# Kernel tuning notes

Hardware: AMD Instinct MI355X
Metric: run time of the kernel (lower is better)

Reference implementation:

```python
import jax, jax.numpy as jnp
import numpy as np

TAU = 1.0
BETA = 1.0


def setup_inputs() -> dict:
    key = jax.random.key(0)
    n, depth = 128, 2048
    inputs = jax.random.normal(key, (1, n, n, depth), dtype=jnp.float32)
    return {"inputs": inputs}


def reference(inputs):
    # Faithful vectorized version of MaskLayer.call (original uses Python loops).
    x = inputs[0]                      # (n, n, d), channels-last feature maps
    n = x.shape[0]
    d = x.shape[2]
    # Per-channel argmax over the flattened (row-major) n*n map.
    flat_idx = jnp.argmax(x.reshape(n * n, d), axis=0)   # (d,)
    # NOTE: original code sets row = idx % n -> i_max, col = idx // n -> j_max
    # (i.e. transposed coordinates); we reproduce that exactly.
    i_max = (flat_idx % n).astype(jnp.float32)           # (d,)
    j_max = (flat_idx // n).astype(jnp.float32)          # (d,)
    i = jnp.arange(n, dtype=jnp.float32)[:, None, None]  # (n,1,1)
    j = jnp.arange(n, dtype=jnp.float32)[None, :, None]  # (1,n,1)
    l1 = jnp.abs(i - i_max) + jnp.abs(j - j_max)         # (n,n,d)
    mask = TAU * jnp.maximum(-1.0, 1.0 - BETA * l1 / n)
    return x * mask
```

## Files before the change

### kernel.cpp

```cpp
#include <hip/hip_runtime.h>

constexpr int N_  = 128;
constexpr int D_  = 2048;
constexpr int NP_ = N_ * N_;

typedef float f32x4 __attribute__((ext_vector_type(4)));

__device__ __forceinline__ unsigned int fmap(float f) {
    unsigned int b = __float_as_uint(f);
    return (b & 0x80000000u) ? ~b : (b | 0x80000000u);
}

__global__ __launch_bounds__(256)
void argmax_kernel(const float* __restrict__ x,
                   unsigned long long* __restrict__ keys) {
    const int cIdx = blockIdx.x * 256 + threadIdx.x;
    const int p0   = blockIdx.y * 64;
    const f32x4* __restrict__ x4 = (const f32x4*)x;

    unsigned long long b0 = 0, b1 = 0, b2 = 0, b3 = 0;
    #pragma unroll 8
    for (int p = p0; p < p0 + 64; ++p) {
        f32x4 v = x4[(size_t)p * (D_ / 4) + cIdx];
        unsigned long long lo = (unsigned long long)(unsigned int)(NP_ - 1 - p);
        unsigned long long k0 = ((unsigned long long)fmap(v.x) << 32) | lo;
        unsigned long long k1 = ((unsigned long long)fmap(v.y) << 32) | lo;
        unsigned long long k2 = ((unsigned long long)fmap(v.z) << 32) | lo;
        unsigned long long k3 = ((unsigned long long)fmap(v.w) << 32) | lo;
        b0 = max(b0, k0);
        b1 = max(b1, k1);
        b2 = max(b2, k2);
        b3 = max(b3, k3);
    }
    unsigned long long* k = keys + (size_t)cIdx * 4;
    atomicMax(&k[0], b0);
    atomicMax(&k[1], b1);
    atomicMax(&k[2], b2);
    atomicMax(&k[3], b3);
}

__global__ __launch_bounds__(256)
void apply_kernel(const float* __restrict__ x,
                  const unsigned long long* __restrict__ keys,
                  float* __restrict__ out) {
    const int g  = blockIdx.x * 256 + threadIdx.x;
    const int e  = g * 4;
    const int c4 = e & (D_ - 1);
    const int p  = e >> 11;
    const float fi = (float)(p >> 7);
    const float fj = (float)(p & 127);

    f32x4 v = __builtin_nontemporal_load(((const f32x4*)x) + g);

    float m[4];
    #pragma unroll
    for (int t = 0; t < 4; ++t) {
        unsigned long long k = keys[c4 + t];
        unsigned int pm = (unsigned int)(NP_ - 1) - (unsigned int)(k & 0xFFFFFFFFull);
        float imax = (float)(pm & 127);
        float jmax = (float)(pm >> 7);
        float l1 = fabsf(fi - imax) + fabsf(fj - jmax);
        m[t] = fmaxf(-1.0f, 1.0f - l1 * (1.0f / 128.0f));
    }

    f32x4 o;
    o.x = v.x * m[0];
    o.y = v.y * m[1];
    o.z = v.z * m[2];
    o.w = v.w * m[3];
    __builtin_nontemporal_store(o, ((f32x4*)out) + g);
}

extern "C" void kernel_launch(void* const* d_in, const int* in_sizes, int n_in,
                              void* d_out, int out_size, void* d_ws, size_t ws_size,
                              hipStream_t stream) {
    const float* x = (const float*)d_in[0];
    float* out = (float*)d_out;
    unsigned long long* keys = (unsigned long long*)d_ws;

    (void)hipMemsetAsync(keys, 0, D_ * sizeof(unsigned long long), stream);

    dim3 g1(2, 256);
    argmax_kernel<<<g1, dim3(256), 0, stream>>>(x, keys);

    const int total4 = NP_ * D_ / 4;
    apply_kernel<<<total4 / 256, dim3(256), 0, stream>>>(x, keys, out);
}
```

Baseline: 257.3 us.

## Replace atomic argmax with two-stage reduction and grid-stride apply kernel

Argmax partials are written per row block and then reduced in a separate small kernel. This removes the memset and 64-bit atomics, and the reduce kernel also precomputes the float max coordinates. The apply kernel becomes a grid-stride loop over 2048 blocks and uses normal rather than nontemporal loads for x, so data cached from the argmax pass may be reused. In exchange it adds an extra kernel launch and a workspace buffer for the partials.

```diff
diff --git a/kernel.cpp b/kernel.cpp
--- a/kernel.cpp
+++ b/kernel.cpp
@@ -3,8 +3,10 @@
 constexpr int N_  = 128;
 constexpr int D_  = 2048;
 constexpr int NP_ = N_ * N_;
+constexpr int YB_ = 256;
 
 typedef float f32x4 __attribute__((ext_vector_type(4)));
+typedef float f32x2 __attribute__((ext_vector_type(2)));
 
 __device__ __forceinline__ unsigned int fmap(float f) {
     unsigned int b = __float_as_uint(f);
@@ -12,15 +14,16 @@
 }
 
 __global__ __launch_bounds__(256)
-void argmax_kernel(const float* __restrict__ x,
-                   unsigned long long* __restrict__ keys) {
+void argmax_partial(const float* __restrict__ x,
+                    unsigned long long* __restrict__ partial) {
     const int cIdx = blockIdx.x * 256 + threadIdx.x;
-    const int p0   = blockIdx.y * 64;
+    const int by   = blockIdx.y;
+    const int p0   = by * (NP_ / YB_);
     const f32x4* __restrict__ x4 = (const f32x4*)x;
 
     unsigned long long b0 = 0, b1 = 0, b2 = 0, b3 = 0;
     #pragma unroll 8
-    for (int p = p0; p < p0 + 64; ++p) {
+    for (int p = p0; p < p0 + (NP_ / YB_); ++p) {
         f32x4 v = x4[(size_t)p * (D_ / 4) + cIdx];
         unsigned long long lo = (unsigned long long)(unsigned int)(NP_ - 1 - p);
         unsigned long long k0 = ((unsigned long long)fmap(v.x) << 32) | lo;
@@ -32,43 +35,49 @@
         b2 = max(b2, k2);
         b3 = max(b3, k3);
     }
-    unsigned long long* k = keys + (size_t)cIdx * 4;
-    atomicMax(&k[0], b0);
-    atomicMax(&k[1], b1);
-    atomicMax(&k[2], b2);
-    atomicMax(&k[3], b3);
+    unsigned long long* dst = partial + (size_t)by * D_ + (size_t)cIdx * 4;
+    dst[0] = b0; dst[1] = b1; dst[2] = b2; dst[3] = b3;
+}
+
+__global__ __launch_bounds__(64)
+void argmax_reduce(const unsigned long long* __restrict__ partial,
+                   f32x2* __restrict__ maxpos) {
+    const int c = blockIdx.x * 64 + threadIdx.x;
+    unsigned long long b = 0;
+    #pragma unroll 8
+    for (int by = 0; by < YB_; ++by)
+        b = max(b, partial[(size_t)by * D_ + c]);
+    unsigned int pm = (unsigned int)(NP_ - 1) - (unsigned int)(b & 0xFFFFFFFFull);
+    f32x2 mp;
+    mp.x = (float)(pm & 127);
+    mp.y = (float)(pm >> 7);
+    maxpos[c] = mp;
 }
 
 __global__ __launch_bounds__(256)
 void apply_kernel(const float* __restrict__ x,
-                  const unsigned long long* __restrict__ keys,
+                  const f32x2* __restrict__ maxpos,
                   float* __restrict__ out) {
-    const int g  = blockIdx.x * 256 + threadIdx.x;
-    const int e  = g * 4;
-    const int c4 = e & (D_ - 1);
-    const int p  = e >> 11;
-    const float fi = (float)(p >> 7);
-    const float fj = (float)(p & 127);
+    constexpr int TOTAL4 = NP_ * D_ / 4;
+    constexpr int STRIDE = 2048 * 256;
+    for (int g = blockIdx.x * 256 + threadIdx.x; g < TOTAL4; g += STRIDE) {
+        const int e  = g * 4;
+        const int c4 = e & (D_ - 1);
+        const int p  = e >> 11;
+        const float fi = (float)(p >> 7);
+        const float fj = (float)(p & 127);
 
-    f32x4 v = __builtin_nontemporal_load(((const f32x4*)x) + g);
-
-    float m[4];
-    #pragma unroll
-    for (int t = 0; t < 4; ++t) {
-        unsigned long long k = keys[c4 + t];
-        unsigned int pm = (unsigned int)(NP_ - 1) - (unsigned int)(k & 0xFFFFFFFFull);
-        float imax = (float)(pm & 127);
-        float jmax = (float)(pm >> 7);
-        float l1 = fabsf(fi - imax) + fabsf(fj - jmax);
-        m[t] = fmaxf(-1.0f, 1.0f - l1 * (1.0f / 128.0f));
+        f32x4 v = ((const f32x4*)x)[g];
+        f32x4 o;
+        #pragma unroll
+        for (int t = 0; t < 4; ++t) {
+            f32x2 mp = maxpos[c4 + t];
+            float l1 = fabsf(fi - mp.x) + fabsf(fj - mp.y);
+            float m  = fmaxf(-1.0f, 1.0f - l1 * (1.0f / 128.0f));
+            o[t] = v[t] * m;
+        }
+        __builtin_nontemporal_store(o, ((f32x4*)out) + g);
     }
-
-    f32x4 o;
-    o.x = v.x * m[0];
-    o.y = v.y * m[1];
-    o.z = v.z * m[2];
-    o.w = v.w * m[3];
-    __builtin_nontemporal_store(o, ((f32x4*)out) + g);
 }
 
 extern "C" void kernel_launch(void* const* d_in, const int* in_sizes, int n_in,
@@ -76,13 +85,10 @@
                               hipStream_t stream) {
     const float* x = (const float*)d_in[0];
     float* out = (float*)d_out;
-    unsigned long long* keys = (unsigned long long*)d_ws;
+    unsigned long long* partial = (unsigned long long*)d_ws;
+    f32x2* maxpos = (f32x2*)((char*)d_ws + (size_t)YB_ * D_ * sizeof(unsigned long long));
 
-    (void)hipMemsetAsync(keys, 0, D_ * sizeof(unsigned long long), stream);
-
-    dim3 g1(2, 256);
-    argmax_kernel<<<g1, dim3(256), 0, stream>>>(x, keys);
-
-    const int total4 = NP_ * D_ / 4;
-    apply_kernel<<<total4 / 256, dim3(256), 0, stream>>>(x, keys, out);
+    argmax_partial<<<dim3(2, YB_), dim3(256), 0, stream>>>(x, partial);
+    argmax_reduce<<<dim3(32), dim3(64), 0, stream>>>(partial, maxpos);
+    apply_kernel<<<dim3(2048), dim3(256), 0, stream>>>(x, maxpos, out);
 }
```

Measured after the change: 260.5 us. Within noise of the previous version (+1.2%).
